# Kernel optimization log

Hardware: AMD Instinct MI355X
Metric: run time of the kernel (lower is better)

## Reference

```python
import jax, jax.numpy as jnp
import numpy as np

D_IN = 512
D_OUT = 512


def setup_inputs() -> dict:
    key = jax.random.key(0)
    ks = jax.random.split(key, 7)
    B, S = 4, 4096
    sc = 1.0 / np.sqrt(D_IN)
    return {
        "x": jax.random.normal(ks[0], (B, S, D_IN), dtype=jnp.float32),
        "Wq": jax.random.normal(ks[1], (D_IN, D_OUT), dtype=jnp.float32) * sc,
        "bq": jnp.zeros((D_OUT,), dtype=jnp.float32),
        "Wk": jax.random.normal(ks[2], (D_IN, D_OUT), dtype=jnp.float32) * sc,
        "bk": jnp.zeros((D_OUT,), dtype=jnp.float32),
        "Wv": jax.random.normal(ks[3], (D_IN, D_OUT), dtype=jnp.float32) * sc,
        "bv": jnp.zeros((D_OUT,), dtype=jnp.float32),
    }


def reference(x, Wq, bq, Wk, bk, Wv, bv):
    # Linear projections
    Q = x @ Wq + bq  # [B,S,Do]
    K = x @ Wk + bk
    V = x @ Wv + bv
    # NOTE: original torch code computes `len(K) ** 1 / 2` which is
    # (len(K)**1)/2 = batch_size / 2 due to operator precedence (not sqrt).
    scale = x.shape[0] / 2.0
    scores = jnp.einsum("bsd,btd->bst", Q, K) / scale  # [B,S,S]
    a = jax.nn.softmax(scores, axis=-1)
    Z = jnp.einsum("bst,btd->bsd", a, V)  # [B,S,Do]
    return Z
```

## Files before the change

kernel.cpp:

```cpp
#include <hip/hip_runtime.h>

typedef _Float16 h8 __attribute__((ext_vector_type(8)));
typedef float f4 __attribute__((ext_vector_type(4)));

#define MFMA16(a, b, c) __builtin_amdgcn_mfma_f32_16x16x32_f16((a), (b), (c), 0, 0, 0)

__device__ static inline void gl_lds16(const void* g, void* l) {
  __builtin_amdgcn_global_load_lds((const __attribute__((address_space(1))) unsigned int*)g,
                                   (__attribute__((address_space(3))) unsigned int*)l, 16, 0, 0);
}


__global__ void wconv_kernel(const float* __restrict__ Wq, const float* __restrict__ Wk,
                             const float* __restrict__ Wv, _Float16* __restrict__ Wt) {
  int idx = blockIdx.x * 256 + threadIdx.x;
  int z = idx >> 15, rem = idx & 32767;
  int n = rem >> 6, k0 = (rem & 63) << 3;
  const float* W = (z == 0) ? Wq : (z == 1) ? Wk : Wv;
  float sc = (z == 0) ? 0.5f : 1.0f;
  h8 v;
#pragma unroll
  for (int j = 0; j < 8; ++j) v[j] = (_Float16)(W[(k0 + j) * 512 + n] * sc);
  size_t blk = (size_t)((z * 4 + (n >> 7)) * 8 + (k0 >> 6));
  int off = (n & 127) * 64 + ((((k0 >> 3) & 7) ^ (n & 7)) << 3);
  *(h8*)&Wt[blk * 8192 + off] = v;
}

__global__ __launch_bounds__(256, 3)
void proj_kernel(const float* __restrict__ x, const _Float16* __restrict__ Wt,
                 const float* __restrict__ bq, const float* __restrict__ bk,
                 const float* __restrict__ bv,
                 char* __restrict__ Qimg, char* __restrict__ Kimg, char* __restrict__ VTimg) {
  __shared__ _Float16 sMem[16384];
  _Float16* sA = sMem;
  _Float16* sB = sMem + 8192;
  const int tid = threadIdx.x;
  const int wave = tid >> 6, lane = tid & 63;
  const int quad = lane >> 4, lr = lane & 15;
  const int mbase = blockIdx.x * 128, nbase = blockIdx.y * 128, z = blockIdx.z;
  const int sr = tid >> 1, sseg = tid & 1;
  const int rbase = (wave & 1) * 64, cbase = (wave >> 1) * 64;
  const char* WtB = (const char*)Wt + ((size_t)(z * 4 + (nbase >> 7)) * 8) * 16384;

  float4 ax[8];
  f4 acc[4][4];
#pragma unroll
  for (int i = 0; i < 4; ++i)
#pragma unroll
    for (int j = 0; j < 4; ++j) { f4 zz = {0.f, 0.f, 0.f, 0.f}; acc[i][j] = zz; }

  {
    const float4* asrc = (const float4*)&x[(size_t)(mbase + sr) * 512 + sseg * 32];
#pragma unroll
    for (int i = 0; i < 8; ++i) ax[i] = asrc[i];
#pragma unroll
    for (int j = 0; j < 4; ++j)
      gl_lds16(WtB + tid * 16 + j * 4096, (char*)sB + tid * 16 + j * 4096);
  }

  for (int kt = 0; kt < 8; ++kt) {
    if (kt > 0) __syncthreads();
#pragma unroll
    for (int i = 0; i < 4; ++i) {
      h8 v;
      float4 f0 = ax[2 * i], f1 = ax[2 * i + 1];
      v[0] = (_Float16)f0.x; v[1] = (_Float16)f0.y; v[2] = (_Float16)f0.z; v[3] = (_Float16)f0.w;
      v[4] = (_Float16)f1.x; v[5] = (_Float16)f1.y; v[6] = (_Float16)f1.z; v[7] = (_Float16)f1.w;
      *(h8*)&sA[sr * 64 + (((sseg * 4 + i) ^ (sr & 7)) << 3)] = v;
    }
    if (kt > 0) {
#pragma unroll
      for (int j = 0; j < 4; ++j)
        gl_lds16(WtB + kt * 16384 + tid * 16 + j * 4096, (char*)sB + tid * 16 + j * 4096);
    }
    __syncthreads();
    if (kt < 7) {
      const float4* asrc = (const float4*)&x[(size_t)(mbase + sr) * 512 + (kt + 1) * 64 + sseg * 32];
#pragma unroll
      for (int i = 0; i < 8; ++i) ax[i] = asrc[i];
    }
#pragma unroll
    for (int ks = 0; ks < 2; ++ks) {
      h8 a[4], bb[4];
#pragma unroll
      for (int rt = 0; rt < 4; ++rt) {
        const int r = rbase + rt * 16 + lr;
        a[rt] = *(const h8*)&sA[r * 64 + ((((ks << 2) | quad) ^ (lr & 7)) << 3)];
      }
#pragma unroll
      for (int ct = 0; ct < 4; ++ct) {
        const int r = cbase + ct * 16 + lr;
        bb[ct] = *(const h8*)&sB[r * 64 + ((((ks << 2) | quad) ^ (lr & 7)) << 3)];
      }
#pragma unroll
      for (int rt = 0; rt < 4; ++rt)
#pragma unroll
        for (int ct = 0; ct < 4; ++ct)
          acc[rt][ct] = MFMA16(a[rt], bb[ct], acc[rt][ct]);
    }
  }

  const float* bias = (z == 0) ? bq : (z == 1) ? bk : bv;
  const float bscale = (z == 0) ? 0.5f : 1.0f;
  _Float16* sC = sMem;
  __syncthreads();
#pragma unroll
  for (int ct = 0; ct < 4; ++ct) {
    const int dl = cbase + ct * 16 + lr;
    const float bb = bias[nbase + dl] * bscale;
#pragma unroll
    for (int rt = 0; rt < 4; ++rt) {
#pragma unroll
      for (int r = 0; r < 4; ++r) {
        const int sl = rbase + rt * 16 + quad * 4 + r;
        const _Float16 val = (_Float16)(acc[rt][ct][r] + bb);
        if (z == 2) {
          sC[((sl >> 6) << 13) + dl * 64 + ((((sl >> 3) & 7) ^ (dl & 7)) << 3) + (sl & 7)] = val;
        } else {
          sC[((dl >> 6) << 13) + sl * 64 + ((((dl >> 3) & 7) ^ (sl & 7)) << 3) + (dl & 7)] = val;
        }
      }
    }
  }
  __syncthreads();
  const int b_ = mbase >> 12;
  char* dst;
  if (z != 2) {
    char* img = (z == 0) ? Qimg : Kimg;
    dst = img + ((size_t)((b_ * 32 + ((mbase & 4095) >> 7)) * 8 + (nbase >> 6) + (tid >> 7))) * 16384;
  } else {
    dst = VTimg + ((size_t)((b_ * 4 + (nbase >> 7)) * 64 + ((mbase & 4095) >> 6) + (tid >> 7))) * 16384;
  }
  dst += (size_t)(tid & 127) * 128;
#pragma unroll
  for (int k = 0; k < 8; ++k)
    *(int4*)(dst + k * 16) = *(const int4*)&sC[tid * 64 + k * 8];
}

__global__ __launch_bounds__(256, 3)
void qk_kernel(const char* __restrict__ Qimg, const char* __restrict__ Kimg,
               char* __restrict__ S, int b0, int s0) {
  __shared__ _Float16 sMem[16384];
  _Float16* sA = sMem;
  _Float16* sB = sMem + 8192;
  const int tid = threadIdx.x;
  const int wave = tid >> 6, lane = tid & 63;
  const int quad = lane >> 4, lr = lane & 15;
  const int cb = blockIdx.x;
  const int rbL = blockIdx.z * gridDim.y + blockIdx.y;
  const int b = b0 + blockIdx.z;
  const int rbase = (wave & 1) * 64, cbase = (wave >> 1) * 64;
  const char* Ab = Qimg + ((size_t)((b * 32 + (s0 >> 7) + blockIdx.y) * 8)) * 16384;
  const char* Bb = Kimg + ((size_t)((b * 32 + cb) * 8)) * 16384;

  f4 acc[4][4];
#pragma unroll
  for (int i = 0; i < 4; ++i)
#pragma unroll
    for (int j = 0; j < 4; ++j) { f4 zz = {0.f, 0.f, 0.f, 0.f}; acc[i][j] = zz; }

#pragma unroll
  for (int j = 0; j < 4; ++j) {
    gl_lds16(Ab + tid * 16 + j * 4096, (char*)sA + tid * 16 + j * 4096);
    gl_lds16(Bb + tid * 16 + j * 4096, (char*)sB + tid * 16 + j * 4096);
  }

  for (int kt = 0; kt < 8; ++kt) {
    __syncthreads();
#pragma unroll
    for (int ks = 0; ks < 2; ++ks) {
      h8 a[4], bb[4];
#pragma unroll
      for (int rt = 0; rt < 4; ++rt) {
        const int r = rbase + rt * 16 + lr;
        a[rt] = *(const h8*)&sA[r * 64 + ((((ks << 2) | quad) ^ (lr & 7)) << 3)];
      }
#pragma unroll
      for (int ct = 0; ct < 4; ++ct) {
        const int r = cbase + ct * 16 + lr;
        bb[ct] = *(const h8*)&sB[r * 64 + ((((ks << 2) | quad) ^ (lr & 7)) << 3)];
      }
#pragma unroll
      for (int rt = 0; rt < 4; ++rt)
#pragma unroll
        for (int ct = 0; ct < 4; ++ct)
          acc[rt][ct] = MFMA16(a[rt], bb[ct], acc[rt][ct]);
    }
    __syncthreads();
    if (kt < 7) {
#pragma unroll
      for (int j = 0; j < 4; ++j) {
        gl_lds16(Ab + (kt + 1) * 16384 + tid * 16 + j * 4096, (char*)sA + tid * 16 + j * 4096);
        gl_lds16(Bb + (kt + 1) * 16384 + tid * 16 + j * 4096, (char*)sB + tid * 16 + j * 4096);
      }
    }
  }

  _Float16* sC = sMem;
#pragma unroll
  for (int ct = 0; ct < 4; ++ct) {
    const int tl = cbase + ct * 16 + lr;
#pragma unroll
    for (int rt = 0; rt < 4; ++rt) {
#pragma unroll
      for (int r = 0; r < 4; ++r) {
        const int sl = rbase + rt * 16 + quad * 4 + r;
        sC[((tl >> 6) << 13) + sl * 64 + ((((tl >> 3) & 7) ^ (sl & 7)) << 3) + (tl & 7)] =
            (_Float16)acc[rt][ct][r];
      }
    }
  }
  __syncthreads();
  char* dst = S + ((size_t)(rbL * 64 + cb * 2 + (tid >> 7))) * 16384 + (size_t)(tid & 127) * 128;
#pragma unroll
  for (int k = 0; k < 8; ++k)
    *(int4*)(dst + k * 16) = *(const int4*)&sC[tid * 64 + k * 8];
}

__global__ __launch_bounds__(256, 2)
void ml_kernel(char* __restrict__ S, float* __restrict__ linv, int b0, int s0, int msLog) {
  const int tid = threadIdx.x;
  const int wave = tid >> 6, lane = tid & 63;
  const int r = blockIdx.x * 4 + wave;
  const int rbL = r >> 7, rl = r & 127;
  char* base = S + ((size_t)(rbL * 64 + lane)) * 16384 + (size_t)rl * 128;
  h8 v[8];
#pragma unroll
  for (int k = 0; k < 8; ++k) v[k] = *(const h8*)(base + k * 16);
  float m = -3.0e38f;
#pragma unroll
  for (int k = 0; k < 8; ++k)
#pragma unroll
    for (int j = 0; j < 8; ++j) m = fmaxf(m, (float)v[k][j]);
  m = fmaxf(m, __shfl_xor(m, 1));
  m = fmaxf(m, __shfl_xor(m, 2));
  m = fmaxf(m, __shfl_xor(m, 4));
  m = fmaxf(m, __shfl_xor(m, 8));
  m = fmaxf(m, __shfl_xor(m, 16));
  m = fmaxf(m, __shfl_xor(m, 32));
  float s = 0.f;
#pragma unroll
  for (int k = 0; k < 8; ++k)
#pragma unroll
    for (int j = 0; j < 8; ++j) {
      float e = __expf((float)v[k][j] - m);
      v[k][j] = (_Float16)e;
      s += e;
    }
#pragma unroll
  for (int k = 0; k < 8; ++k) *(h8*)(base + k * 16) = v[k];
  s += __shfl_xor(s, 1);
  s += __shfl_xor(s, 2);
  s += __shfl_xor(s, 4);
  s += __shfl_xor(s, 8);
  s += __shfl_xor(s, 16);
  s += __shfl_xor(s, 32);
  if (lane == 0) {
    const int bL = r >> msLog, sloc = r & ((1 << msLog) - 1);
    linv[(b0 + bL) * 4096 + s0 + sloc] = 1.0f / s;
  }
}

__global__ __launch_bounds__(256, 4)
void pv_kernel(const char* __restrict__ S, const char* __restrict__ VTimg,
               const float* __restrict__ linv, float* __restrict__ out, int b0, int s0) {
  __shared__ _Float16 sMem[12288];
  _Float16* sA = sMem;
  _Float16* sB = sMem + 4096;
  const int tid = threadIdx.x;
  const int wave = tid >> 6, lane = tid & 63;
  const int quad = lane >> 4, lr = lane & 15;
  const int db = blockIdx.x;
  const int sbL = blockIdx.z * gridDim.y + blockIdx.y;
  const int b = b0 + blockIdx.z;
  const int rbase = (wave & 1) * 32, cbase = (wave >> 1) * 64;
  const char* Ab = S + ((size_t)((sbL >> 1) * 64)) * 16384 + (size_t)(sbL & 1) * 8192;
  const char* Bb = VTimg + ((size_t)((b * 4 + db) * 64)) * 16384;

  f4 acc[2][4];
#pragma unroll
  for (int i = 0; i < 2; ++i)
#pragma unroll
    for (int j = 0; j < 4; ++j) { f4 zz = {0.f, 0.f, 0.f, 0.f}; acc[i][j] = zz; }

  {
#pragma unroll
    for (int j = 0; j < 2; ++j)
      gl_lds16(Ab + tid * 16 + j * 4096, (char*)sA + tid * 16 + j * 4096);
#pragma unroll
    for (int j = 0; j < 4; ++j)
      gl_lds16(Bb + tid * 16 + j * 4096, (char*)sB + tid * 16 + j * 4096);
  }

  for (int kt = 0; kt < 64; ++kt) {
    __syncthreads();
#pragma unroll
    for (int ks = 0; ks < 2; ++ks) {
      h8 a[2], bb[4];
#pragma unroll
      for (int rt = 0; rt < 2; ++rt) {
        const int r = rbase + rt * 16 + lr;
        a[rt] = *(const h8*)&sA[r * 64 + ((((ks << 2) | quad) ^ (lr & 7)) << 3)];
      }
#pragma unroll
      for (int ct = 0; ct < 4; ++ct) {
        const int r = cbase + ct * 16 + lr;
        bb[ct] = *(const h8*)&sB[r * 64 + ((((ks << 2) | quad) ^ (lr & 7)) << 3)];
      }
#pragma unroll
      for (int rt = 0; rt < 2; ++rt)
#pragma unroll
        for (int ct = 0; ct < 4; ++ct)
          acc[rt][ct] = MFMA16(a[rt], bb[ct], acc[rt][ct]);
    }
    __syncthreads();
    if (kt < 63) {
#pragma unroll
      for (int j = 0; j < 2; ++j)
        gl_lds16(Ab + (kt + 1) * 16384 + tid * 16 + j * 4096, (char*)sA + tid * 16 + j * 4096);
#pragma unroll
      for (int j = 0; j < 4; ++j)
        gl_lds16(Bb + (kt + 1) * 16384 + tid * 16 + j * 4096, (char*)sB + tid * 16 + j * 4096);
    }
  }

#pragma unroll
  for (int rt = 0; rt < 2; ++rt) {
#pragma unroll
    for (int r = 0; r < 4; ++r) {
      const int srow = s0 + blockIdx.y * 64 + rbase + rt * 16 + quad * 4 + r;
      const float li = linv[b * 4096 + srow];
      float* op = &out[((size_t)b * 4096 + srow) * 512 + db * 128];
#pragma unroll
      for (int ct = 0; ct < 4; ++ct)
        op[cbase + ct * 16 + lr] = acc[rt][ct][r] * li;
    }
  }
}

extern "C" void kernel_launch(void* const* d_in, const int* in_sizes, int n_in,
                              void* d_out, int out_size, void* d_ws, size_t ws_size,
                              hipStream_t stream) {
  (void)in_sizes; (void)n_in; (void)out_size;
  const float* x  = (const float*)d_in[0];
  const float* Wq = (const float*)d_in[1];
  const float* bq = (const float*)d_in[2];
  const float* Wk = (const float*)d_in[3];
  const float* bk = (const float*)d_in[4];
  const float* Wv = (const float*)d_in[5];
  const float* bv = (const float*)d_in[6];
  float* out = (float*)d_out;
  char* ws = (char*)d_ws;
  char* Qimg  = ws;
  char* Kimg  = ws + ((size_t)16 << 20);
  char* VTimg = ws + ((size_t)32 << 20);
  _Float16* Wt = (_Float16*)(ws + ((size_t)48 << 20));
  float* linv  = (float*)(ws + ((size_t)50 << 20) - 65536);
  char* Simg   = ws + ((size_t)50 << 20);

  wconv_kernel<<<dim3(384), dim3(256), 0, stream>>>(Wq, Wk, Wv, Wt);
  proj_kernel<<<dim3(128, 4, 3), dim3(256), 0, stream>>>(x, Wt, bq, bk, bv, Qimg, Kimg, VTimg);

  const size_t avail = ws_size > ((size_t)50 << 20) ? ws_size - ((size_t)50 << 20) : 0;
  int nchunk, nb, Ms;
  if      (avail >= ((size_t)128 << 20)) { nchunk = 1;  nb = 4; Ms = 4096; }
  else if (avail >= ((size_t)64  << 20)) { nchunk = 2;  nb = 2; Ms = 4096; }
  else if (avail >= ((size_t)32  << 20)) { nchunk = 4;  nb = 1; Ms = 4096; }
  else if (avail >= ((size_t)16  << 20)) { nchunk = 8;  nb = 1; Ms = 2048; }
  else if (avail >= ((size_t)8   << 20)) { nchunk = 16; nb = 1; Ms = 1024; }
  else                                   { nchunk = 32; nb = 1; Ms = 512;  }
  int msLog = 31 - __builtin_clz(Ms);
  const int chunksPerBatch = 4096 / Ms;

  for (int c = 0; c < nchunk; ++c) {
    int b0, s0;
    if (nb > 1 || Ms == 4096) { b0 = c * nb; s0 = 0; }
    else { b0 = c / chunksPerBatch; s0 = (c % chunksPerBatch) * Ms; }
    qk_kernel<<<dim3(32, Ms / 128, nb), dim3(256), 0, stream>>>(Qimg, Kimg, Simg, b0, s0);
    ml_kernel<<<dim3(nb * Ms / 4), dim3(256), 0, stream>>>(Simg, linv, b0, s0, msLog);
    pv_kernel<<<dim3(4, Ms / 64, nb), dim3(256), 0, stream>>>(Simg, VTimg, linv, out, b0, s0);
  }
}
```

Measured before the change: 410.7 us.

## Restructure QK GEMM into 256x256 tiles with 8 waves and double-buffered LDS pipeline

The QK^T score kernel now computes 256x256 output tiles with 512-thread blocks instead of 128x128 with 256 threads. It double-buffers Q/K tiles in 128KB of LDS and interleaves async global-to-LDS staging with four MFMA phases per k-step, using explicit waitcnt, barriers and s_setprio. The aim is to raise operand reuse per loaded byte and hide global-load latency behind matrix-core work. The cost is much higher LDS use (one or two blocks per CU) and fragile hand-counted vmcnt synchronisation.

```diff
diff --git a/kernel.cpp b/kernel.cpp
--- a/kernel.cpp
+++ b/kernel.cpp
@@ -137,85 +137,164 @@
     *(int4*)(dst + k * 16) = *(const int4*)&sC[tid * 64 + k * 8];
 }
 
-__global__ __launch_bounds__(256, 3)
+#define STAGE(src, slot)                                                        \
+  gl_lds16((src) + tid * 16, (char*)sMem + (slot) * 16384 + tid * 16);          \
+  gl_lds16((src) + tid * 16 + 8192, (char*)sMem + (slot) * 16384 + tid * 16 + 8192)
+
+__global__ __launch_bounds__(512, 2)
 void qk_kernel(const char* __restrict__ Qimg, const char* __restrict__ Kimg,
                char* __restrict__ S, int b0, int s0) {
-  __shared__ _Float16 sMem[16384];
-  _Float16* sA = sMem;
-  _Float16* sB = sMem + 8192;
+  __shared__ _Float16 sMem[65536];
   const int tid = threadIdx.x;
   const int wave = tid >> 6, lane = tid & 63;
   const int quad = lane >> 4, lr = lane & 15;
+  const int wm = wave >> 2, wn = wave & 3;
   const int cb = blockIdx.x;
   const int rbL = blockIdx.z * gridDim.y + blockIdx.y;
   const int b = b0 + blockIdx.z;
-  const int rbase = (wave & 1) * 64, cbase = (wave >> 1) * 64;
-  const char* Ab = Qimg + ((size_t)((b * 32 + (s0 >> 7) + blockIdx.y) * 8)) * 16384;
-  const char* Bb = Kimg + ((size_t)((b * 32 + cb) * 8)) * 16384;
-
-  f4 acc[4][4];
-#pragma unroll
-  for (int i = 0; i < 4; ++i)
-#pragma unroll
-    for (int j = 0; j < 4; ++j) { f4 zz = {0.f, 0.f, 0.f, 0.f}; acc[i][j] = zz; }
-
-#pragma unroll
-  for (int j = 0; j < 4; ++j) {
-    gl_lds16(Ab + tid * 16 + j * 4096, (char*)sA + tid * 16 + j * 4096);
-    gl_lds16(Bb + tid * 16 + j * 4096, (char*)sB + tid * 16 + j * 4096);
-  }
-
+  const int qrb = (s0 >> 7) + blockIdx.y * 2;
+
+  const char* Ab0 = Qimg + ((size_t)((b * 32 + qrb) * 8)) * 16384;
+  const char* Ab1 = Ab0 + 8 * 16384;
+  const char* Bb0 = Kimg + ((size_t)((b * 32 + cb * 2) * 8)) * 16384;
+  const char* Bb1 = Bb0 + 8 * 16384;
+
+  _Float16* const sBslot = sMem + (wn >> 1) * 8192;
+  _Float16* const sAslot = sMem + (2 + wm) * 8192;
+  const int arow = lr;
+  const int bcol = (wn & 1) * 64 + lr;
+  const int sw = lr & 7;
+
+  STAGE(Bb0, 0); STAGE(Bb1, 1); STAGE(Ab0, 2); STAGE(Ab1, 3);
+  asm volatile("s_waitcnt vmcnt(4)" ::: "memory");
+  STAGE(Bb0 + 16384, 4); STAGE(Bb1 + 16384, 5); STAGE(Ab0 + 16384, 6);
+  asm volatile("s_waitcnt vmcnt(6)" ::: "memory");
+  __builtin_amdgcn_s_barrier();
+  __builtin_amdgcn_sched_barrier(0);
+
+  f4 acc[2][2][4][2];
+#pragma unroll
+  for (int i = 0; i < 2; ++i)
+#pragma unroll
+    for (int j = 0; j < 2; ++j)
+#pragma unroll
+      for (int rt = 0; rt < 4; ++rt)
+#pragma unroll
+        for (int ct = 0; ct < 2; ++ct) { f4 zz = {0.f, 0.f, 0.f, 0.f}; acc[i][j][rt][ct] = zz; }
+  h8 a[4][2], bb[4][2];
+
+#pragma unroll
   for (int kt = 0; kt < 8; ++kt) {
-    __syncthreads();
-#pragma unroll
-    for (int ks = 0; ks < 2; ++ks) {
-      h8 a[4], bb[4];
-#pragma unroll
-      for (int rt = 0; rt < 4; ++rt) {
-        const int r = rbase + rt * 16 + lr;
-        a[rt] = *(const h8*)&sA[r * 64 + ((((ks << 2) | quad) ^ (lr & 7)) << 3)];
-      }
-#pragma unroll
-      for (int ct = 0; ct < 4; ++ct) {
-        const int r = cbase + ct * 16 + lr;
-        bb[ct] = *(const h8*)&sB[r * 64 + ((((ks << 2) | quad) ^ (lr & 7)) << 3)];
-      }
+    const int sb = (kt & 1) * 32768;
+
+#pragma unroll
+    for (int rt = 0; rt < 4; ++rt)
+#pragma unroll
+      for (int ks = 0; ks < 2; ++ks)
+        a[rt][ks] = *(const h8*)&sAslot[sb + (rt * 16 + arow) * 64 + (((ks * 4 + quad) ^ sw) << 3)];
+#pragma unroll
+    for (int ct = 0; ct < 4; ++ct)
+#pragma unroll
+      for (int ks = 0; ks < 2; ++ks)
+        bb[ct][ks] = *(const h8*)&sBslot[sb + (ct * 16 + bcol) * 64 + (((ks * 4 + quad) ^ sw) << 3)];
+    if (kt < 7) { STAGE(Ab1 + (kt + 1) * 16384, ((kt + 1) & 1) * 4 + 3); }
+    __builtin_amdgcn_s_barrier();
+    asm volatile("s_waitcnt lgkmcnt(0)" ::: "memory");
+    __builtin_amdgcn_sched_barrier(0);
+    __builtin_amdgcn_s_setprio(1);
+#pragma unroll
+    for (int rt = 0; rt < 4; ++rt)
+#pragma unroll
+      for (int ct = 0; ct < 2; ++ct)
+#pragma unroll
+        for (int ks = 0; ks < 2; ++ks)
+          acc[0][0][rt][ct] = MFMA16(a[rt][ks], bb[ct][ks], acc[0][0][rt][ct]);
+    __builtin_amdgcn_s_setprio(0);
+    __builtin_amdgcn_s_barrier();
+
+    if (kt < 6) { STAGE(Bb0 + (kt + 2) * 16384, (kt & 1) * 4 + 0); }
+    __builtin_amdgcn_s_barrier();
+    __builtin_amdgcn_s_setprio(1);
+#pragma unroll
+    for (int rt = 0; rt < 4; ++rt)
+#pragma unroll
+      for (int ct = 0; ct < 2; ++ct)
+#pragma unroll
+        for (int ks = 0; ks < 2; ++ks)
+          acc[0][1][rt][ct] = MFMA16(a[rt][ks], bb[2 + ct][ks], acc[0][1][rt][ct]);
+    __builtin_amdgcn_s_setprio(0);
+    __builtin_amdgcn_s_barrier();
+
+#pragma unroll
+    for (int rt = 0; rt < 4; ++rt)
+#pragma unroll
+      for (int ks = 0; ks < 2; ++ks)
+        a[rt][ks] = *(const h8*)&sAslot[sb + (64 + rt * 16 + arow) * 64 + (((ks * 4 + quad) ^ sw) << 3)];
+    if (kt < 6) { STAGE(Bb1 + (kt + 2) * 16384, (kt & 1) * 4 + 1); }
+    __builtin_amdgcn_s_barrier();
+    asm volatile("s_waitcnt lgkmcnt(0)" ::: "memory");
+    __builtin_amdgcn_sched_barrier(0);
+    __builtin_amdgcn_s_setprio(1);
+#pragma unroll
+    for (int rt = 0; rt < 4; ++rt)
+#pragma unroll
+      for (int ct = 0; ct < 2; ++ct)
+#pragma unroll
+        for (int ks = 0; ks < 2; ++ks)
+          acc[1][0][rt][ct] = MFMA16(a[rt][ks], bb[ct][ks], acc[1][0][rt][ct]);
+    __builtin_amdgcn_s_setprio(0);
+    __builtin_amdgcn_s_barrier();
+
+    if (kt < 6) { STAGE(Ab0 + (kt + 2) * 16384, (kt & 1) * 4 + 2); }
+    __builtin_amdgcn_s_barrier();
+    __builtin_amdgcn_s_setprio(1);
+#pragma unroll
+    for (int rt = 0; rt < 4; ++rt)
+#pragma unroll
+      for (int ct = 0; ct < 2; ++ct)
+#pragma unroll
+        for (int ks = 0; ks < 2; ++ks)
+          acc[1][1][rt][ct] = MFMA16(a[rt][ks], bb[2 + ct][ks], acc[1][1][rt][ct]);
+    __builtin_amdgcn_s_setprio(0);
+    if (kt < 6) {
+      asm volatile("s_waitcnt vmcnt(6)" ::: "memory");
+    } else if (kt == 6) {
+      asm volatile("s_waitcnt vmcnt(0)" ::: "memory");
+    }
+    __builtin_amdgcn_s_barrier();
+    __builtin_amdgcn_sched_barrier(0);
+  }
+
+  __syncthreads();
+  _Float16* sC = sMem;
+#pragma unroll
+  for (int mh = 0; mh < 2; ++mh)
+#pragma unroll
+    for (int nh = 0; nh < 2; ++nh)
 #pragma unroll
       for (int rt = 0; rt < 4; ++rt)
 #pragma unroll
-        for (int ct = 0; ct < 4; ++ct)
-          acc[rt][ct] = MFMA16(a[rt], bb[ct], acc[rt][ct]);
-    }
-    __syncthreads();
-    if (kt < 7) {
-#pragma unroll
-      for (int j = 0; j < 4; ++j) {
-        gl_lds16(Ab + (kt + 1) * 16384 + tid * 16 + j * 4096, (char*)sA + tid * 16 + j * 4096);
-        gl_lds16(Bb + (kt + 1) * 16384 + tid * 16 + j * 4096, (char*)sB + tid * 16 + j * 4096);
-      }
-    }
-  }
-
-  _Float16* sC = sMem;
-#pragma unroll
-  for (int ct = 0; ct < 4; ++ct) {
-    const int tl = cbase + ct * 16 + lr;
-#pragma unroll
-    for (int rt = 0; rt < 4; ++rt) {
-#pragma unroll
-      for (int r = 0; r < 4; ++r) {
-        const int sl = rbase + rt * 16 + quad * 4 + r;
-        sC[((tl >> 6) << 13) + sl * 64 + ((((tl >> 3) & 7) ^ (sl & 7)) << 3) + (tl & 7)] =
-            (_Float16)acc[rt][ct][r];
-      }
-    }
-  }
+        for (int ct = 0; ct < 2; ++ct)
+#pragma unroll
+          for (int rr = 0; rr < 4; ++rr) {
+            const int row = wm * 128 + mh * 64 + rt * 16 + quad * 4 + rr;
+            const int col = wn * 64 + nh * 32 + ct * 16 + lr;
+            const int ib = ((row >> 7) << 2) + (col >> 6);
+            const int rw = row & 127, kk = col & 63;
+            sC[ib * 8192 + rw * 64 + ((((kk >> 3) & 7) ^ (rw & 7)) << 3) + (kk & 7)] =
+                (_Float16)acc[mh][nh][rt][ct][rr];
+          }
   __syncthreads();
-  char* dst = S + ((size_t)(rbL * 64 + cb * 2 + (tid >> 7))) * 16384 + (size_t)(tid & 127) * 128;
-#pragma unroll
-  for (int k = 0; k < 8; ++k)
-    *(int4*)(dst + k * 16) = *(const int4*)&sC[tid * 64 + k * 8];
-}
+  const int ib = tid >> 6, tl_ = tid & 63;
+  char* dst = S + ((size_t)((rbL * 2 + (ib >> 2)) * 64 + cb * 4 + (ib & 3))) * 16384;
+#pragma unroll
+  for (int r2 = 0; r2 < 2; ++r2)
+#pragma unroll
+    for (int k = 0; k < 8; ++k)
+      *(int4*)(dst + (tl_ * 2 + r2) * 128 + k * 16) =
+          *(const int4*)&sC[ib * 8192 + (tl_ * 2 + r2) * 64 + k * 8];
+}
+#undef STAGE
 
 __global__ __launch_bounds__(256, 2)
 void ml_kernel(char* __restrict__ S, float* __restrict__ linv, int b0, int s0, int msLog) {
@@ -376,7 +455,7 @@
     int b0, s0;
     if (nb > 1 || Ms == 4096) { b0 = c * nb; s0 = 0; }
     else { b0 = c / chunksPerBatch; s0 = (c % chunksPerBatch) * Ms; }
-    qk_kernel<<<dim3(32, Ms / 128, nb), dim3(256), 0, stream>>>(Qimg, Kimg, Simg, b0, s0);
+    qk_kernel<<<dim3(16, Ms / 256, nb), dim3(512), 0, stream>>>(Qimg, Kimg, Simg, b0, s0);
     ml_kernel<<<dim3(nb * Ms / 4), dim3(256), 0, stream>>>(Simg, linv, b0, s0, msLog);
     pv_kernel<<<dim3(4, Ms / 64, nb), dim3(256), 0, stream>>>(Simg, VTimg, linv, out, b0, s0);
   }
```

After: 429.1 us. 1.04x slower.

## Fuse softmax into QK and PV kernels using atomic row max

Applied to the files above, without the earlier changes.

Removes the separate softmax pass over the score matrix. The QK kernel now reduces each row's max from its accumulators and publishes it with an atomicMax on an order-preserving unsigned encoding. The PV kernel reads the raw fp16 scores, applies exp(s - max) while staging the A tile into LDS, accumulates row sums, and normalises at the end. This saves a full read-modify-write of S and one launch, but PV now does exp work on every tile, each of the 4 column blocks recomputes it, and the A tile goes through registers instead of async global-to-LDS loads.

```diff
diff --git a/kernel.cpp b/kernel.cpp
--- a/kernel.cpp
+++ b/kernel.cpp
@@ -10,10 +10,20 @@
                                    (__attribute__((address_space(3))) unsigned int*)l, 16, 0, 0);
 }
 
+__device__ static inline unsigned encf(float f) {
+  unsigned u = __float_as_uint(f);
+  return (u & 0x80000000u) ? ~u : (u | 0x80000000u);
+}
+__device__ static inline float decf(unsigned u) {
+  return __uint_as_float((u & 0x80000000u) ? (u ^ 0x80000000u) : ~u);
+}
+
 
 __global__ void wconv_kernel(const float* __restrict__ Wq, const float* __restrict__ Wk,
-                             const float* __restrict__ Wv, _Float16* __restrict__ Wt) {
+                             const float* __restrict__ Wv, _Float16* __restrict__ Wt,
+                             unsigned* __restrict__ mEnc) {
   int idx = blockIdx.x * 256 + threadIdx.x;
+  if (idx < 16384) mEnc[idx] = 0u;
   int z = idx >> 15, rem = idx & 32767;
   int n = rem >> 6, k0 = (rem & 63) << 3;
   const float* W = (z == 0) ? Wq : (z == 1) ? Wk : Wv;
@@ -139,7 +149,7 @@
 
 __global__ __launch_bounds__(256, 3)
 void qk_kernel(const char* __restrict__ Qimg, const char* __restrict__ Kimg,
-               char* __restrict__ S, int b0, int s0) {
+               char* __restrict__ S, unsigned* __restrict__ mEnc, int b0, int s0) {
   __shared__ _Float16 sMem[16384];
   _Float16* sA = sMem;
   _Float16* sB = sMem + 8192;
@@ -196,6 +206,24 @@
     }
   }
 
+  {
+    const int growb = b * 4096 + s0 + blockIdx.y * 128;
+#pragma unroll
+    for (int rt = 0; rt < 4; ++rt) {
+#pragma unroll
+      for (int r = 0; r < 4; ++r) {
+        float mx = fmaxf(fmaxf(acc[rt][0][r], acc[rt][1][r]),
+                         fmaxf(acc[rt][2][r], acc[rt][3][r]));
+        mx = fmaxf(mx, __shfl_xor(mx, 1));
+        mx = fmaxf(mx, __shfl_xor(mx, 2));
+        mx = fmaxf(mx, __shfl_xor(mx, 4));
+        mx = fmaxf(mx, __shfl_xor(mx, 8));
+        if (lr == 0)
+          atomicMax(&mEnc[growb + rbase + rt * 16 + quad * 4 + r], encf(mx));
+      }
+    }
+  }
+
   _Float16* sC = sMem;
 #pragma unroll
   for (int ct = 0; ct < 4; ++ct) {
@@ -217,54 +245,11 @@
     *(int4*)(dst + k * 16) = *(const int4*)&sC[tid * 64 + k * 8];
 }
 
-__global__ __launch_bounds__(256, 2)
-void ml_kernel(char* __restrict__ S, float* __restrict__ linv, int b0, int s0, int msLog) {
-  const int tid = threadIdx.x;
-  const int wave = tid >> 6, lane = tid & 63;
-  const int r = blockIdx.x * 4 + wave;
-  const int rbL = r >> 7, rl = r & 127;
-  char* base = S + ((size_t)(rbL * 64 + lane)) * 16384 + (size_t)rl * 128;
-  h8 v[8];
-#pragma unroll
-  for (int k = 0; k < 8; ++k) v[k] = *(const h8*)(base + k * 16);
-  float m = -3.0e38f;
-#pragma unroll
-  for (int k = 0; k < 8; ++k)
-#pragma unroll
-    for (int j = 0; j < 8; ++j) m = fmaxf(m, (float)v[k][j]);
-  m = fmaxf(m, __shfl_xor(m, 1));
-  m = fmaxf(m, __shfl_xor(m, 2));
-  m = fmaxf(m, __shfl_xor(m, 4));
-  m = fmaxf(m, __shfl_xor(m, 8));
-  m = fmaxf(m, __shfl_xor(m, 16));
-  m = fmaxf(m, __shfl_xor(m, 32));
-  float s = 0.f;
-#pragma unroll
-  for (int k = 0; k < 8; ++k)
-#pragma unroll
-    for (int j = 0; j < 8; ++j) {
-      float e = __expf((float)v[k][j] - m);
-      v[k][j] = (_Float16)e;
-      s += e;
-    }
-#pragma unroll
-  for (int k = 0; k < 8; ++k) *(h8*)(base + k * 16) = v[k];
-  s += __shfl_xor(s, 1);
-  s += __shfl_xor(s, 2);
-  s += __shfl_xor(s, 4);
-  s += __shfl_xor(s, 8);
-  s += __shfl_xor(s, 16);
-  s += __shfl_xor(s, 32);
-  if (lane == 0) {
-    const int bL = r >> msLog, sloc = r & ((1 << msLog) - 1);
-    linv[(b0 + bL) * 4096 + s0 + sloc] = 1.0f / s;
-  }
-}
-
 __global__ __launch_bounds__(256, 4)
 void pv_kernel(const char* __restrict__ S, const char* __restrict__ VTimg,
-               const float* __restrict__ linv, float* __restrict__ out, int b0, int s0) {
+               const unsigned* __restrict__ mEnc, float* __restrict__ out, int b0, int s0) {
   __shared__ _Float16 sMem[12288];
+  __shared__ float ls[64];
   _Float16* sA = sMem;
   _Float16* sB = sMem + 4096;
   const int tid = threadIdx.x;
@@ -277,6 +262,12 @@
   const char* Ab = S + ((size_t)((sbL >> 1) * 64)) * 16384 + (size_t)(sbL & 1) * 8192;
   const char* Bb = VTimg + ((size_t)((b * 4 + db) * 64)) * 16384;
 
+  const int lrow = tid >> 3;
+  const int growb = b * 4096 + s0 + blockIdx.y * 64;
+  const float m0 = decf(mEnc[growb + lrow]);
+  const float m1 = decf(mEnc[growb + 32 + lrow]);
+  float rs0 = 0.f, rs1 = 0.f;
+
   f4 acc[2][4];
 #pragma unroll
   for (int i = 0; i < 2; ++i)
@@ -284,12 +275,23 @@
     for (int j = 0; j < 4; ++j) { f4 zz = {0.f, 0.f, 0.f, 0.f}; acc[i][j] = zz; }
 
   {
-#pragma unroll
-    for (int j = 0; j < 2; ++j)
-      gl_lds16(Ab + tid * 16 + j * 4096, (char*)sA + tid * 16 + j * 4096);
 #pragma unroll
     for (int j = 0; j < 4; ++j)
       gl_lds16(Bb + tid * 16 + j * 4096, (char*)sB + tid * 16 + j * 4096);
+    {
+      h8 ha = *(const h8*)(Ab + tid * 16);
+      h8 w;
+#pragma unroll
+      for (int u = 0; u < 8; ++u) { float e = __expf((float)ha[u] - m0); w[u] = (_Float16)e; rs0 += e; }
+      *(h8*)((char*)sA + tid * 16) = w;
+    }
+    {
+      h8 ha = *(const h8*)(Ab + tid * 16 + 4096);
+      h8 w;
+#pragma unroll
+      for (int u = 0; u < 8; ++u) { float e = __expf((float)ha[u] - m1); w[u] = (_Float16)e; rs1 += e; }
+      *(h8*)((char*)sA + tid * 16 + 4096) = w;
+    }
   }
 
   for (int kt = 0; kt < 64; ++kt) {
@@ -316,20 +318,37 @@
     __syncthreads();
     if (kt < 63) {
 #pragma unroll
-      for (int j = 0; j < 2; ++j)
-        gl_lds16(Ab + (kt + 1) * 16384 + tid * 16 + j * 4096, (char*)sA + tid * 16 + j * 4096);
-#pragma unroll
       for (int j = 0; j < 4; ++j)
         gl_lds16(Bb + (kt + 1) * 16384 + tid * 16 + j * 4096, (char*)sB + tid * 16 + j * 4096);
-    }
-  }
+      {
+        h8 ha = *(const h8*)(Ab + (kt + 1) * 16384 + tid * 16);
+        h8 w;
+#pragma unroll
+        for (int u = 0; u < 8; ++u) { float e = __expf((float)ha[u] - m0); w[u] = (_Float16)e; rs0 += e; }
+        *(h8*)((char*)sA + tid * 16) = w;
+      }
+      {
+        h8 ha = *(const h8*)(Ab + (kt + 1) * 16384 + tid * 16 + 4096);
+        h8 w;
+#pragma unroll
+        for (int u = 0; u < 8; ++u) { float e = __expf((float)ha[u] - m1); w[u] = (_Float16)e; rs1 += e; }
+        *(h8*)((char*)sA + tid * 16 + 4096) = w;
+      }
+    }
+  }
+
+  rs0 += __shfl_xor(rs0, 1); rs0 += __shfl_xor(rs0, 2); rs0 += __shfl_xor(rs0, 4);
+  rs1 += __shfl_xor(rs1, 1); rs1 += __shfl_xor(rs1, 2); rs1 += __shfl_xor(rs1, 4);
+  if ((tid & 7) == 0) { ls[lrow] = rs0; ls[32 + lrow] = rs1; }
+  __syncthreads();
 
 #pragma unroll
   for (int rt = 0; rt < 2; ++rt) {
 #pragma unroll
     for (int r = 0; r < 4; ++r) {
-      const int srow = s0 + blockIdx.y * 64 + rbase + rt * 16 + quad * 4 + r;
-      const float li = linv[b * 4096 + srow];
+      const int lrw = rbase + rt * 16 + quad * 4 + r;
+      const int srow = s0 + blockIdx.y * 64 + lrw;
+      const float li = 1.0f / ls[lrw];
       float* op = &out[((size_t)b * 4096 + srow) * 512 + db * 128];
 #pragma unroll
       for (int ct = 0; ct < 4; ++ct)
@@ -355,10 +374,10 @@
   char* Kimg  = ws + ((size_t)16 << 20);
   char* VTimg = ws + ((size_t)32 << 20);
   _Float16* Wt = (_Float16*)(ws + ((size_t)48 << 20));
-  float* linv  = (float*)(ws + ((size_t)50 << 20) - 65536);
+  unsigned* mEnc = (unsigned*)(ws + ((size_t)50 << 20) - 65536);
   char* Simg   = ws + ((size_t)50 << 20);
 
-  wconv_kernel<<<dim3(384), dim3(256), 0, stream>>>(Wq, Wk, Wv, Wt);
+  wconv_kernel<<<dim3(384), dim3(256), 0, stream>>>(Wq, Wk, Wv, Wt, mEnc);
   proj_kernel<<<dim3(128, 4, 3), dim3(256), 0, stream>>>(x, Wt, bq, bk, bv, Qimg, Kimg, VTimg);
 
   const size_t avail = ws_size > ((size_t)50 << 20) ? ws_size - ((size_t)50 << 20) : 0;
@@ -369,15 +388,13 @@
   else if (avail >= ((size_t)16  << 20)) { nchunk = 8;  nb = 1; Ms = 2048; }
   else if (avail >= ((size_t)8   << 20)) { nchunk = 16; nb = 1; Ms = 1024; }
   else                                   { nchunk = 32; nb = 1; Ms = 512;  }
-  int msLog = 31 - __builtin_clz(Ms);
   const int chunksPerBatch = 4096 / Ms;
 
   for (int c = 0; c < nchunk; ++c) {
     int b0, s0;
     if (nb > 1 || Ms == 4096) { b0 = c * nb; s0 = 0; }
     else { b0 = c / chunksPerBatch; s0 = (c % chunksPerBatch) * Ms; }
-    qk_kernel<<<dim3(32, Ms / 128, nb), dim3(256), 0, stream>>>(Qimg, Kimg, Simg, b0, s0);
-    ml_kernel<<<dim3(nb * Ms / 4), dim3(256), 0, stream>>>(Simg, linv, b0, s0, msLog);
-    pv_kernel<<<dim3(4, Ms / 64, nb), dim3(256), 0, stream>>>(Simg, VTimg, linv, out, b0, s0);
-  }
-}
+    qk_kernel<<<dim3(32, Ms / 128, nb), dim3(256), 0, stream>>>(Qimg, Kimg, Simg, mEnc, b0, s0);
+    pv_kernel<<<dim3(4, Ms / 64, nb), dim3(256), 0, stream>>>(Simg, VTimg, mEnc, out, b0, s0);
+  }
+}
```

Result: faster. 375.9 us (-8.5%).
